# Performance work log

Measured on AMD Instinct MI355X. Metric: run time of the kernel, lower is better.

The kernel has to match this reference:

```python
import jax, jax.numpy as jnp
from jax import lax
import numpy as np

B, C, H, W = 2, 64, 128, 128
DN = ('NCHW', 'OIHW', 'NCHW')


def setup_inputs() -> dict:
    key = jax.random.key(0)
    ks = jax.random.split(key, 20)
    rn = lambda k, s, sc=0.05: jax.random.normal(k, s, dtype=jnp.float32) * sc
    inp = {
        'x': jax.random.normal(ks[0], (B, C, H, W), dtype=jnp.float32),
        'off1_w': rn(ks[1], (C, 1, 1, 15)), 'off1_b': rn(ks[2], (C,)),
        'bn1_s': 1.0 + rn(ks[3], (C,)), 'bn1_b': rn(ks[4], (C,)),
        'off2_w': rn(ks[5], (C, 1, 15, 1)), 'off2_b': rn(ks[6], (C,)),
        'bn2_s': 1.0 + rn(ks[7], (C,)), 'bn2_b': rn(ks[8], (C,)),
        'off3_w': rn(ks[9], (C, 1, 3, 3)), 'off3_b': rn(ks[10], (C,)),
        'bn3_s': 1.0 + rn(ks[11], (C,)), 'bn3_b': rn(ks[12], (C,)),
        'bal_w': rn(ks[13], (18, C, 1, 1)), 'bal_b': rn(ks[14], (18,)),
        'bn4_s': 1.0 + rn(ks[15], (18,)), 'bn4_b': rn(ks[16], (18,)),
        'dw2': rn(ks[17], (C, 1, 3, 3), 0.1),
        'dw3': rn(jax.random.fold_in(key, 101), (C, 1, 3, 3), 0.1),
        'dw4': rn(jax.random.fold_in(key, 102), (C, 1, 3, 3), 0.1),
        'dw5': rn(jax.random.fold_in(key, 103), (C, 1, 3, 3), 0.1),
        'fin_w': rn(ks[18], (C, C, 1, 1)), 'fin_b': rn(ks[19], (C,)),
        'bn5_s': 1.0 + rn(jax.random.fold_in(key, 104), (C,)),
        'bn5_b': rn(jax.random.fold_in(key, 105), (C,)),
    }
    return inp


def _dwconv(x, w, pad):
    return lax.conv_general_dilated(x, w, (1, 1), [(pad[0], pad[0]), (pad[1], pad[1])],
                                    dimension_numbers=DN, feature_group_count=x.shape[1])


def _conv1x1(x, w):
    return lax.conv_general_dilated(x, w, (1, 1), 'VALID', dimension_numbers=DN)


def _bias(x, b):
    return x + b[None, :, None, None]


def _bn(x, s, b):  # inference-form BatchNorm folded into per-channel affine
    return x * s[None, :, None, None] + b[None, :, None, None]


def _bilinear(x, py, px):
    # x: [B,C,H,W]; py/px: [B,9,H,W] float sampling coords -> [B,C,9,H,W]
    Bn, Cn, Hn, Wn = x.shape
    y0 = jnp.floor(py)
    x0 = jnp.floor(px)
    wy1 = py - y0  # fractional parts
    wx1 = px - x0
    xf = x.reshape(Bn, Cn, Hn * Wn)

    def gather(yi, xi):
        valid = (yi >= 0) & (yi <= Hn - 1) & (xi >= 0) & (xi <= Wn - 1)
        yc = jnp.clip(yi, 0, Hn - 1).astype(jnp.int32)
        xc = jnp.clip(xi, 0, Wn - 1).astype(jnp.int32)
        idx = (yc * Wn + xc).reshape(Bn, -1)  # [B, 9*H*W]
        v = jax.vmap(lambda f, i: f[:, i])(xf, idx)  # [B,C,9*H*W]
        v = v.reshape(Bn, Cn, 9, Hn, Wn)
        return v * valid[:, None].astype(x.dtype)  # zero padding outside

    g00 = gather(y0, x0)
    g01 = gather(y0, x0 + 1)
    g10 = gather(y0 + 1, x0)
    g11 = gather(y0 + 1, x0 + 1)
    wy1e = wy1[:, None]
    wx1e = wx1[:, None]
    return (g00 * (1 - wy1e) * (1 - wx1e) + g01 * (1 - wy1e) * wx1e
            + g10 * wy1e * (1 - wx1e) + g11 * wy1e * wx1e)


def _deform_dw(x, offsets, w, d):
    # depthwise DeformConv2d: kernel 3x3, stride 1, padding=d, dilation=d, groups=C
    Bn, Cn, Hn, Wn = x.shape
    off = offsets.reshape(Bn, 9, 2, Hn, Wn)  # pairs (dy, dx) per kernel tap, row-major
    ky = (jnp.arange(9) // 3 - 1).astype(x.dtype)  # [-1,-1,-1,0,0,0,1,1,1]
    kx = (jnp.arange(9) % 3 - 1).astype(x.dtype)
    hs = jnp.arange(Hn, dtype=x.dtype)
    ws = jnp.arange(Wn, dtype=x.dtype)
    # output loc h maps to input h - pad + ki*dil = h + (ki-1)*d since pad == dil == d
    py = off[:, :, 0] + (hs[:, None] + d * ky[:, None, None])[None]  # [B,9,H,W]
    px = off[:, :, 1] + (ws[None, :] + d * kx[:, None, None])[None]
    s = _bilinear(x, py, px)  # [B,C,9,H,W]
    return jnp.einsum('bckhw,ck->bchw', s, w.reshape(Cn, 9))


def reference(x, off1_w, off1_b, bn1_s, bn1_b, off2_w, off2_b, bn2_s, bn2_b,
              off3_w, off3_b, bn3_s, bn3_b, bal_w, bal_b, bn4_s, bn4_b,
              dw2, dw3, dw4, dw5, fin_w, fin_b, bn5_s, bn5_b):
    # DirectionOffsets: three depthwise convs + BN, summed, then 1x1 -> 18ch + BN
    o1 = _bn(_bias(_dwconv(x, off1_w, (0, 7)), off1_b), bn1_s, bn1_b)
    o2 = _bn(_bias(_dwconv(x, off2_w, (7, 0)), off2_b), bn2_s, bn2_b)
    o3 = _bn(_bias(_dwconv(x, off3_w, (1, 1)), off3_b), bn3_s, bn3_b)
    off = _bn(_bias(_conv1x1(o1 + o2 + o3, bal_w), bal_b), bn4_s, bn4_b)  # [B,18,H,W]
    # four deformable depthwise convs sharing the offset field
    out = (_deform_dw(x, off, dw2, 2) + _deform_dw(x, off, dw3, 3)
           + _deform_dw(x, off, dw4, 4) + _deform_dw(x, off, dw5, 5))
    out = _bn(_bias(_conv1x1(out, fin_w), fin_b), bn5_s, bn5_b) * x
    return out
```

## Files before the change

kernel.cpp:

```cpp
#include <hip/hip_runtime.h>

#define BB 2
#define CC 64
#define HH 128
#define WW 128
#define HWN (HH*WW)
#define CHW (CC*HWN)

#define BAND_H 8
#define HALO   8
#define NBAND  (HH / BAND_H)
#define LROWS  (BAND_H + 2 * HALO)
#define CPB    2
#define XPAD   8
#define XSTR   (WW + 2 * XPAD)

#define OB_H 16
#define OB_HALO 7
#define OB_ROWS (OB_H + 2 * OB_HALO)
#define OSTR 144

__global__ __launch_bounds__(256) void osum_kernel(const float* __restrict__ x,
    const float* __restrict__ w1, const float* __restrict__ b1, const float* __restrict__ s1, const float* __restrict__ g1,
    const float* __restrict__ w2, const float* __restrict__ b2, const float* __restrict__ s2, const float* __restrict__ g2,
    const float* __restrict__ w3, const float* __restrict__ b3, const float* __restrict__ s3, const float* __restrict__ g3,
    float* __restrict__ osum)
{
    __shared__ float xs[OB_ROWS * OSTR];
    int bid  = blockIdx.x;
    int band = bid & 7;
    int bc   = bid >> 3;
    int c    = bc & (CC - 1);
    int bs   = band * OB_H;
    int r_lo_v = bs - OB_HALO;

    for (int i = threadIdx.x; i < (OB_ROWS * OSTR) / 4; i += 256)
        ((float4*)xs)[i] = make_float4(0.f, 0.f, 0.f, 0.f);
    __syncthreads();

    int gstart = r_lo_v < 0 ? 0 : r_lo_v;
    int gend   = r_lo_v + OB_ROWS; if (gend > HH) gend = HH;
    int nitems = (gend - gstart) * (WW / 4);
    const float* xp = x + (size_t)bc * HWN;
    for (int i = threadIdx.x; i < nitems; i += 256) {
        int r = i >> 5, col4 = i & 31;
        int g = gstart + r;
        int lr = g - r_lo_v;
        ((float4*)xs)[lr * (OSTR / 4) + 2 + col4] = ((const float4*)(xp + g * WW))[col4];
    }
    __syncthreads();

    float W1[15], W2[15], W3[9];
    #pragma unroll
    for (int k = 0; k < 15; ++k) { W1[k] = w1[c * 15 + k]; W2[k] = w2[c * 15 + k]; }
    #pragma unroll
    for (int k = 0; k < 9; ++k) W3[k] = w3[c * 9 + k];
    float bb1 = b1[c], ss1 = s1[c], gg1 = g1[c];
    float bb2 = b2[c], ss2 = s2[c], gg2 = g2[c];
    float bb3 = b3[c], ss3 = s3[c], gg3 = g3[c];

    const float4* XS4 = (const float4*)xs;
    int oct = threadIdx.x & 15;
    int row = threadIdx.x >> 4;
    int w0  = oct * 8;
    int lr  = row + OB_HALO;
    int h   = bs + row;

    float hb[24];
    #pragma unroll
    for (int t = 0; t < 6; ++t) {
        float4 q = XS4[lr * (OSTR / 4) + 2 * oct + t];
        hb[4*t] = q.x; hb[4*t+1] = q.y; hb[4*t+2] = q.z; hb[4*t+3] = q.w;
    }
    float a1[8];
    #pragma unroll
    for (int j = 0; j < 8; ++j) {
        float s = 0.f;
        #pragma unroll
        for (int k = 0; k < 15; ++k) s += hb[j + 1 + k] * W1[k];
        a1[j] = s;
    }

    float a2[8] = {0.f,0.f,0.f,0.f,0.f,0.f,0.f,0.f};
    #pragma unroll
    for (int k = 0; k < 15; ++k) {
        float4 qa = XS4[(lr + k - 7) * (OSTR / 4) + 2 + 2 * oct];
        float4 qb = XS4[(lr + k - 7) * (OSTR / 4) + 3 + 2 * oct];
        a2[0] += qa.x * W2[k]; a2[1] += qa.y * W2[k]; a2[2] += qa.z * W2[k]; a2[3] += qa.w * W2[k];
        a2[4] += qb.x * W2[k]; a2[5] += qb.y * W2[k]; a2[6] += qb.z * W2[k]; a2[7] += qb.w * W2[k];
    }

    float a3[8] = {0.f,0.f,0.f,0.f,0.f,0.f,0.f,0.f};
    #pragma unroll
    for (int kh = 0; kh < 3; ++kh) {
        float m[16];
        #pragma unroll
        for (int t = 0; t < 4; ++t) {
            float4 q = XS4[(lr + kh - 1) * (OSTR / 4) + 1 + 2 * oct + t];
            m[4*t] = q.x; m[4*t+1] = q.y; m[4*t+2] = q.z; m[4*t+3] = q.w;
        }
        #pragma unroll
        for (int j = 0; j < 8; ++j)
            #pragma unroll
            for (int kw = 0; kw < 3; ++kw)
                a3[j] += m[j + kw + 3] * W3[kh * 3 + kw];
    }

    float o[8];
    #pragma unroll
    for (int j = 0; j < 8; ++j)
        o[j] = (a1[j] + bb1) * ss1 + gg1
             + (a2[j] + bb2) * ss2 + gg2
             + (a3[j] + bb3) * ss3 + gg3;
    float* dst = osum + (size_t)bc * HWN + h * WW + w0;
    ((float4*)dst)[0] = make_float4(o[0], o[1], o[2], o[3]);
    ((float4*)dst)[1] = make_float4(o[4], o[5], o[6], o[7]);
}

__global__ __launch_bounds__(256) void off_kernel(const float* __restrict__ osum,
    const float* __restrict__ balw, const float* __restrict__ balb,
    const float* __restrict__ s4, const float* __restrict__ g4,
    float* __restrict__ off)
{
    __shared__ float ls[CC * 64];
    int bid = blockIdx.x;
    int b   = bid >> 8;
    int hw0 = (bid & 255) * 64;

    const float* src = osum + (size_t)b * CHW + hw0;
    #pragma unroll
    for (int i = 0; i < 4; ++i) {
        int idx = threadIdx.x + i * 256;
        int row = idx >> 4, col4 = idx & 15;
        ((float4*)ls)[row * 16 + col4] = *(const float4*)(src + (size_t)row * HWN + col4 * 4);
    }
    __syncthreads();

    int px = threadIdx.x & 63;
    int og = __builtin_amdgcn_readfirstlane((int)(threadIdx.x >> 6));
    int start = (og < 2) ? og * 5 : 10 + (og - 2) * 4;
    int cnt   = (og < 2) ? 5 : 4;

    float acc[5] = {0.f, 0.f, 0.f, 0.f, 0.f};
    for (int ic = 0; ic < CC; ++ic) {
        float v = ls[ic * 64 + px];
        #pragma unroll
        for (int j = 0; j < 5; ++j)
            if (j < cnt) acc[j] += v * balw[(start + j) * CC + ic];
    }
    #pragma unroll
    for (int j = 0; j < 5; ++j)
        if (j < cnt) {
            int oc = start + j;
            off[(size_t)b * (18 * HWN) + (size_t)oc * HWN + hw0 + px] =
                (acc[j] + balb[oc]) * s4[oc] + g4[oc];
        }
}

__device__ __forceinline__ float gz(const float* __restrict__ xp, int y, int x) {
    return ((unsigned)y < (unsigned)HH && (unsigned)x < (unsigned)WW) ? xp[y * WW + x] : 0.f;
}

__global__ __launch_bounds__(256) void deform_kernel(
    const float* __restrict__ x,
    const float* __restrict__ off,
    const float* __restrict__ dw2, const float* __restrict__ dw3,
    const float* __restrict__ dw4, const float* __restrict__ dw5,
    float* __restrict__ pre)
{
    __shared__ float xs[LROWS * XSTR * CPB];

    int bid  = blockIdx.x;
    int band = bid & (NBAND - 1);
    int bcp  = bid >> 4;
    int cp   = bcp & 31;
    int b    = bcp >> 5;
    int c0   = cp * CPB;
    int bc0  = b * CC + c0;

    int r_lo_v = band * BAND_H - HALO;

    for (int i = threadIdx.x; i < (LROWS * XSTR * CPB) / 4; i += 256)
        ((float4*)xs)[i] = make_float4(0.f, 0.f, 0.f, 0.f);
    __syncthreads();

    int gstart = r_lo_v < 0 ? 0 : r_lo_v;
    int gend   = r_lo_v + LROWS; if (gend > HH) gend = HH;
    int nitems = (gend - gstart) * (WW / 4);
    const float* xp0 = x + (size_t)bc0 * HWN;
    const float* xp1 = xp0 + HWN;
    for (int i = threadIdx.x; i < nitems; i += 256) {
        int r = i >> 5, col4 = i & 31;
        int g = gstart + r;
        int lr = g - r_lo_v;
        float4 q0 = ((const float4*)(xp0 + g * WW))[col4];
        float4 q1 = ((const float4*)(xp1 + g * WW))[col4];
        ((float4*)xs)[lr * (XSTR / 2) + XPAD / 2 + col4 * 2]     = make_float4(q0.x, q1.x, q0.y, q1.y);
        ((float4*)xs)[lr * (XSTR / 2) + XPAD / 2 + col4 * 2 + 1] = make_float4(q0.z, q1.z, q0.w, q1.w);
    }
    __syncthreads();

    const float2* XS2 = (const float2*)xs;
    const float* offb = off + (size_t)b * (18 * HWN);

    #pragma unroll 1
    for (int chunk = 0; chunk < (BAND_H * WW) / 256; ++chunk) {
        int p = band * (BAND_H * WW) + chunk * 256 + (int)threadIdx.x;
        float hf = (float)(p >> 7);
        float wf = (float)(p & (WW - 1));

        float oy[9], ox[9];
        #pragma unroll
        for (int k = 0; k < 9; ++k) {
            oy[k] = offb[((size_t)(2 * k) << 14) + p];
            ox[k] = offb[((size_t)(2 * k + 1) << 14) + p];
        }

        float acc0 = 0.f, acc1 = 0.f;
        #pragma unroll
        for (int k = 0; k < 9; ++k) {
            const int ky = k / 3 - 1, kx = k % 3 - 1;
            float pyb = oy[k] + hf;
            float pxb = ox[k] + wf;
            float y0f = floorf(pyb), x0f = floorf(pxb);
            float wy = pyb - y0f, wx = pxb - x0f;
            int y0g = (int)y0f, x0g = (int)x0f;
            int y0b = y0g - r_lo_v;
            int x0b = x0g + XPAD;
            float cxa = 1.f - wx, cxb = wx;

            const int dkyLo = (ky < 0) ? -5 : (ky > 0 ? 2 : 0);
            const int dkyHi = (ky < 0) ? -2 : (ky > 0 ? 5 : 0);
            const int dkxLo = (kx < 0) ? -5 : (kx > 0 ? 2 : 0);
            const int dkxHi = (kx < 0) ? -2 : (kx > 0 ? 5 : 0);
            bool ok = (y0b + dkyLo >= 0) & (y0b + dkyHi <= LROWS - 2)
                    & (x0b + dkxLo >= 0) & (x0b + dkxHi <= XSTR - 2);

            if (ok) {
                #pragma unroll
                for (int di = 0; di < 4; ++di) {
                    const int d = di + 2;
                    int f0 = (y0b + d * ky) * XSTR + (x0b + d * kx);
                    float2 a  = XS2[f0],        bq = XS2[f0 + 1];
                    float2 cq = XS2[f0 + XSTR], dq = XS2[f0 + XSTR + 1];
                    float ra0 = cxa * a.x + cxb * bq.x;
                    float rb0 = cxa * cq.x + cxb * dq.x;
                    float ra1 = cxa * a.y + cxb * bq.y;
                    float rb1 = cxa * cq.y + cxb * dq.y;
                    float s0 = ra0 + wy * (rb0 - ra0);
                    float s1 = ra1 + wy * (rb1 - ra1);
                    const float* dwp = (di == 0) ? dw2 : (di == 1) ? dw3 : (di == 2) ? dw4 : dw5;
                    acc0 += s0 * dwp[c0 * 9 + k];
                    acc1 += s1 * dwp[(c0 + 1) * 9 + k];
                }
            } else {
                #pragma unroll
                for (int di = 0; di < 4; ++di) {
                    const int d = di + 2;
                    int yy = y0g + d * ky, xx = x0g + d * kx;
                    float v00 = gz(xp0, yy, xx),     v01 = gz(xp0, yy, xx + 1);
                    float v10 = gz(xp0, yy + 1, xx), v11 = gz(xp0, yy + 1, xx + 1);
                    float u00 = gz(xp1, yy, xx),     u01 = gz(xp1, yy, xx + 1);
                    float u10 = gz(xp1, yy + 1, xx), u11 = gz(xp1, yy + 1, xx + 1);
                    float s0 = (1.f - wy) * (cxa * v00 + cxb * v01) + wy * (cxa * v10 + cxb * v11);
                    float s1 = (1.f - wy) * (cxa * u00 + cxb * u01) + wy * (cxa * u10 + cxb * u11);
                    const float* dwp = (di == 0) ? dw2 : (di == 1) ? dw3 : (di == 2) ? dw4 : dw5;
                    acc0 += s0 * dwp[c0 * 9 + k];
                    acc1 += s1 * dwp[(c0 + 1) * 9 + k];
                }
            }
        }
        pre[((size_t)bc0 << 14) + p]       = acc0;
        pre[((size_t)(bc0 + 1) << 14) + p] = acc1;
    }
}

__global__ __launch_bounds__(256) void final_kernel(const float* __restrict__ pre,
    const float* __restrict__ finw, const float* __restrict__ finb,
    const float* __restrict__ s5, const float* __restrict__ g5,
    const float* __restrict__ x, float* __restrict__ out)
{
    __shared__ float ls[CC * 64];
    int bid = blockIdx.x;
    int b   = bid >> 8;
    int hw0 = (bid & 255) * 64;

    const float* src = pre + (size_t)b * CHW + hw0;
    #pragma unroll
    for (int i = 0; i < 4; ++i) {
        int idx = threadIdx.x + i * 256;
        int row = idx >> 4, col4 = idx & 15;
        ((float4*)ls)[row * 16 + col4] = *(const float4*)(src + (size_t)row * HWN + col4 * 4);
    }
    __syncthreads();

    int hw = threadIdx.x & 63;
    int og = __builtin_amdgcn_readfirstlane((int)(threadIdx.x >> 6));

    float acc[16];
    #pragma unroll
    for (int j = 0; j < 16; ++j) acc[j] = 0.f;
    for (int ic = 0; ic < CC; ++ic) {
        float v = ls[ic * 64 + hw];
        #pragma unroll
        for (int j = 0; j < 16; ++j)
            acc[j] += v * finw[(og * 16 + j) * CC + ic];
    }
    #pragma unroll
    for (int j = 0; j < 16; ++j) {
        int oc = og * 16 + j;
        size_t oidx = ((size_t)(b * CC + oc) << 14) + hw0 + hw;
        out[oidx] = ((acc[j] + finb[oc]) * s5[oc] + g5[oc]) * x[oidx];
    }
}

extern "C" void kernel_launch(void* const* d_in, const int* in_sizes, int n_in,
                              void* d_out, int out_size, void* d_ws, size_t ws_size,
                              hipStream_t stream) {
    const float* x      = (const float*)d_in[0];
    const float* off1_w = (const float*)d_in[1];
    const float* off1_b = (const float*)d_in[2];
    const float* bn1_s  = (const float*)d_in[3];
    const float* bn1_b  = (const float*)d_in[4];
    const float* off2_w = (const float*)d_in[5];
    const float* off2_b = (const float*)d_in[6];
    const float* bn2_s  = (const float*)d_in[7];
    const float* bn2_b  = (const float*)d_in[8];
    const float* off3_w = (const float*)d_in[9];
    const float* off3_b = (const float*)d_in[10];
    const float* bn3_s  = (const float*)d_in[11];
    const float* bn3_b  = (const float*)d_in[12];
    const float* bal_w  = (const float*)d_in[13];
    const float* bal_b  = (const float*)d_in[14];
    const float* bn4_s  = (const float*)d_in[15];
    const float* bn4_b  = (const float*)d_in[16];
    const float* dw2    = (const float*)d_in[17];
    const float* dw3    = (const float*)d_in[18];
    const float* dw4    = (const float*)d_in[19];
    const float* dw5    = (const float*)d_in[20];
    const float* fin_w  = (const float*)d_in[21];
    const float* fin_b  = (const float*)d_in[22];
    const float* bn5_s  = (const float*)d_in[23];
    const float* bn5_b  = (const float*)d_in[24];

    float* ws   = (float*)d_ws;
    float* osum = ws;
    float* off  = ws + (size_t)BB * CHW;
    float* pre  = off + (size_t)BB * 18 * HWN;

    float* out = (float*)d_out;

    osum_kernel<<<BB * CC * (HH / OB_H), 256, 0, stream>>>(x,
        off1_w, off1_b, bn1_s, bn1_b,
        off2_w, off2_b, bn2_s, bn2_b,
        off3_w, off3_b, bn3_s, bn3_b, osum);
    off_kernel<<<BB * (HWN / 64), 256, 0, stream>>>(osum, bal_w, bal_b, bn4_s, bn4_b, off);
    deform_kernel<<<BB * (CC / CPB) * NBAND, 256, 0, stream>>>(x, off, dw2, dw3, dw4, dw5, pre);
    final_kernel<<<BB * (HWN / 64), 256, 0, stream>>>(pre, fin_w, fin_b, bn5_s, bn5_b, x, out);
}
```

Measured before the change: 164.5 us.

## Interleave offset field as float2 pairs and skip full LDS zeroing for interior bands

Result: no change. 164.0 us (-0.3%).

```diff
diff --git a/kernel.cpp b/kernel.cpp
--- a/kernel.cpp
+++ b/kernel.cpp
@@ -120,7 +120,7 @@
 __global__ __launch_bounds__(256) void off_kernel(const float* __restrict__ osum,
     const float* __restrict__ balw, const float* __restrict__ balb,
     const float* __restrict__ s4, const float* __restrict__ g4,
-    float* __restrict__ off)
+    float2* __restrict__ off2)
 {
     __shared__ float ls[CC * 64];
     int bid = blockIdx.x;
@@ -138,22 +138,29 @@
 
     int px = threadIdx.x & 63;
     int og = __builtin_amdgcn_readfirstlane((int)(threadIdx.x >> 6));
-    int start = (og < 2) ? og * 5 : 10 + (og - 2) * 4;
-    int cnt   = (og < 2) ? 5 : 4;
-
-    float acc[5] = {0.f, 0.f, 0.f, 0.f, 0.f};
+    int np = (og == 0) ? 3 : 2;
+
+    float accy[3] = {0.f, 0.f, 0.f};
+    float accx[3] = {0.f, 0.f, 0.f};
     for (int ic = 0; ic < CC; ++ic) {
         float v = ls[ic * 64 + px];
         #pragma unroll
-        for (int j = 0; j < 5; ++j)
-            if (j < cnt) acc[j] += v * balw[(start + j) * CC + ic];
-    }
-    #pragma unroll
-    for (int j = 0; j < 5; ++j)
-        if (j < cnt) {
-            int oc = start + j;
-            off[(size_t)b * (18 * HWN) + (size_t)oc * HWN + hw0 + px] =
-                (acc[j] + balb[oc]) * s4[oc] + g4[oc];
+        for (int j = 0; j < 3; ++j)
+            if (j < np) {
+                int k = og + j * 4;
+                accy[j] += v * balw[(2 * k)     * CC + ic];
+                accx[j] += v * balw[(2 * k + 1) * CC + ic];
+            }
+    }
+    #pragma unroll
+    for (int j = 0; j < 3; ++j)
+        if (j < np) {
+            int k = og + j * 4;
+            int ocy = 2 * k, ocx = 2 * k + 1;
+            float2 o;
+            o.x = (accy[j] + balb[ocy]) * s4[ocy] + g4[ocy];
+            o.y = (accx[j] + balb[ocx]) * s4[ocx] + g4[ocx];
+            off2[((size_t)b * 9 + k) * HWN + hw0 + px] = o;
         }
 }
 
@@ -163,7 +170,7 @@
 
 __global__ __launch_bounds__(256) void deform_kernel(
     const float* __restrict__ x,
-    const float* __restrict__ off,
+    const float2* __restrict__ off2,
     const float* __restrict__ dw2, const float* __restrict__ dw3,
     const float* __restrict__ dw4, const float* __restrict__ dw5,
     float* __restrict__ pre)
@@ -179,29 +186,46 @@
     int bc0  = b * CC + c0;
 
     int r_lo_v = band * BAND_H - HALO;
-
-    for (int i = threadIdx.x; i < (LROWS * XSTR * CPB) / 4; i += 256)
-        ((float4*)xs)[i] = make_float4(0.f, 0.f, 0.f, 0.f);
-    __syncthreads();
-
-    int gstart = r_lo_v < 0 ? 0 : r_lo_v;
-    int gend   = r_lo_v + LROWS; if (gend > HH) gend = HH;
-    int nitems = (gend - gstart) * (WW / 4);
     const float* xp0 = x + (size_t)bc0 * HWN;
     const float* xp1 = xp0 + HWN;
-    for (int i = threadIdx.x; i < nitems; i += 256) {
-        int r = i >> 5, col4 = i & 31;
-        int g = gstart + r;
-        int lr = g - r_lo_v;
-        float4 q0 = ((const float4*)(xp0 + g * WW))[col4];
-        float4 q1 = ((const float4*)(xp1 + g * WW))[col4];
-        ((float4*)xs)[lr * (XSTR / 2) + XPAD / 2 + col4 * 2]     = make_float4(q0.x, q1.x, q0.y, q1.y);
-        ((float4*)xs)[lr * (XSTR / 2) + XPAD / 2 + col4 * 2 + 1] = make_float4(q0.z, q1.z, q0.w, q1.w);
-    }
-    __syncthreads();
+
+    bool interior = (r_lo_v >= 0) && (r_lo_v + LROWS <= HH);
+    if (interior) {
+        if (threadIdx.x < 192) {
+            int lr = threadIdx.x >> 3, q = threadIdx.x & 7;
+            int tc = (q < 4) ? q : 64 + q;
+            ((float4*)xs)[lr * (XSTR / 2) + tc] = make_float4(0.f, 0.f, 0.f, 0.f);
+        }
+        for (int i = threadIdx.x; i < LROWS * (WW / 4); i += 256) {
+            int r = i >> 5, col4 = i & 31;
+            int g = r_lo_v + r;
+            float4 q0 = ((const float4*)(xp0 + g * WW))[col4];
+            float4 q1 = ((const float4*)(xp1 + g * WW))[col4];
+            ((float4*)xs)[r * (XSTR / 2) + XPAD / 2 + col4 * 2]     = make_float4(q0.x, q1.x, q0.y, q1.y);
+            ((float4*)xs)[r * (XSTR / 2) + XPAD / 2 + col4 * 2 + 1] = make_float4(q0.z, q1.z, q0.w, q1.w);
+        }
+        __syncthreads();
+    } else {
+        for (int i = threadIdx.x; i < (LROWS * XSTR * CPB) / 4; i += 256)
+            ((float4*)xs)[i] = make_float4(0.f, 0.f, 0.f, 0.f);
+        __syncthreads();
+        int gstart = r_lo_v < 0 ? 0 : r_lo_v;
+        int gend   = r_lo_v + LROWS; if (gend > HH) gend = HH;
+        int nitems = (gend - gstart) * (WW / 4);
+        for (int i = threadIdx.x; i < nitems; i += 256) {
+            int r = i >> 5, col4 = i & 31;
+            int g = gstart + r;
+            int lr = g - r_lo_v;
+            float4 q0 = ((const float4*)(xp0 + g * WW))[col4];
+            float4 q1 = ((const float4*)(xp1 + g * WW))[col4];
+            ((float4*)xs)[lr * (XSTR / 2) + XPAD / 2 + col4 * 2]     = make_float4(q0.x, q1.x, q0.y, q1.y);
+            ((float4*)xs)[lr * (XSTR / 2) + XPAD / 2 + col4 * 2 + 1] = make_float4(q0.z, q1.z, q0.w, q1.w);
+        }
+        __syncthreads();
+    }
 
     const float2* XS2 = (const float2*)xs;
-    const float* offb = off + (size_t)b * (18 * HWN);
+    const float2* offb = off2 + (size_t)b * 9 * HWN;
 
     #pragma unroll 1
     for (int chunk = 0; chunk < (BAND_H * WW) / 256; ++chunk) {
@@ -209,19 +233,17 @@
         float hf = (float)(p >> 7);
         float wf = (float)(p & (WW - 1));
 
-        float oy[9], ox[9];
-        #pragma unroll
-        for (int k = 0; k < 9; ++k) {
-            oy[k] = offb[((size_t)(2 * k) << 14) + p];
-            ox[k] = offb[((size_t)(2 * k + 1) << 14) + p];
-        }
+        float2 ofk[9];
+        #pragma unroll
+        for (int k = 0; k < 9; ++k)
+            ofk[k] = offb[(size_t)k * HWN + p];
 
         float acc0 = 0.f, acc1 = 0.f;
         #pragma unroll
         for (int k = 0; k < 9; ++k) {
             const int ky = k / 3 - 1, kx = k % 3 - 1;
-            float pyb = oy[k] + hf;
-            float pxb = ox[k] + wf;
+            float pyb = ofk[k].x + hf;
+            float pxb = ofk[k].y + wf;
             float y0f = floorf(pyb), x0f = floorf(pxb);
             float wy = pyb - y0f, wx = pxb - x0f;
             int y0g = (int)y0f, x0g = (int)x0f;
@@ -237,12 +259,13 @@
                     & (x0b + dkxLo >= 0) & (x0b + dkxHi <= XSTR - 2);
 
             if (ok) {
+                const float2* pb = XS2 + (y0b * XSTR + x0b);
                 #pragma unroll
                 for (int di = 0; di < 4; ++di) {
-                    const int d = di + 2;
-                    int f0 = (y0b + d * ky) * XSTR + (x0b + d * kx);
-                    float2 a  = XS2[f0],        bq = XS2[f0 + 1];
-                    float2 cq = XS2[f0 + XSTR], dq = XS2[f0 + XSTR + 1];
+                    const int d  = di + 2;
+                    const int st = d * (ky * XSTR + kx);
+                    float2 a  = pb[st],        bq = pb[st + 1];
+                    float2 cq = pb[st + XSTR], dq = pb[st + XSTR + 1];
                     float ra0 = cxa * a.x + cxb * bq.x;
                     float rb0 = cxa * cq.x + cxb * dq.x;
                     float ra1 = cxa * a.y + cxb * bq.y;
@@ -345,8 +368,8 @@
 
     float* ws   = (float*)d_ws;
     float* osum = ws;
-    float* off  = ws + (size_t)BB * CHW;
-    float* pre  = off + (size_t)BB * 18 * HWN;
+    float2* off2 = (float2*)(ws + (size_t)BB * CHW);
+    float* pre  = ws + (size_t)BB * CHW + (size_t)BB * 18 * HWN;
 
     float* out = (float*)d_out;
 
@@ -354,7 +377,7 @@
         off1_w, off1_b, bn1_s, bn1_b,
         off2_w, off2_b, bn2_s, bn2_b,
         off3_w, off3_b, bn3_s, bn3_b, osum);
-    off_kernel<<<BB * (HWN / 64), 256, 0, stream>>>(osum, bal_w, bal_b, bn4_s, bn4_b, off);
-    deform_kernel<<<BB * (CC / CPB) * NBAND, 256, 0, stream>>>(x, off, dw2, dw3, dw4, dw5, pre);
+    off_kernel<<<BB * (HWN / 64), 256, 0, stream>>>(osum, bal_w, bal_b, bn4_s, bn4_b, off2);
+    deform_kernel<<<BB * (CC / CPB) * NBAND, 256, 0, stream>>>(x, off2, dw2, dw3, dw4, dw5, pre);
     final_kernel<<<BB * (HWN / 64), 256, 0, stream>>>(pre, fin_w, fin_b, bn5_s, bn5_b, x, out);
 }
```
